# Performance work log

Measured on AMD Instinct MI355X. Metric: run time of the kernel, lower is better.

## Reference

```python
import jax, jax.numpy as jnp
import numpy as np
from math import log2

FPS = 100.0
MIN_BPM = 55.0
MAX_BPM = 215.0
NUM_TEMPI = 60
NUM_BEATS = 4
TRANS_LAMBDA = 100.0
OBS_LAMBDA = 16.0
NUM_FRAMES = 6000


def _intervals():
    mi = 60.0 * FPS / MAX_BPM
    ma = 60.0 * FPS / MIN_BPM
    iv = np.arange(round(mi), round(ma) + 1)
    if NUM_TEMPI < len(iv):
        n = NUM_TEMPI
        iv = np.zeros(0)
        while len(iv) < NUM_TEMPI:
            iv = np.unique(np.round(np.logspace(log2(mi), log2(ma), n, base=2)))
            n += 1
    return iv.astype(np.int64)


def _state_space():
    iv = _intervals()                      # (I,) tempo intervals in frames
    nsb = int(iv.sum())                    # states per beat
    first = np.concatenate([[0], np.cumsum(iv)[:-1]]).astype(np.int64)
    last = (np.cumsum(iv) - 1).astype(np.int64)
    pos_b = np.concatenate([np.arange(i) / float(i) for i in iv])
    positions = np.concatenate([pos_b + b for b in range(NUM_BEATS)])  # (S,)
    first_states = np.stack([first + b * nsb for b in range(NUM_BEATS)])  # (B,I)
    last_states = np.stack([last + b * nsb for b in range(NUM_BEATS)])    # (B,I)
    # exponential tempo transition (madmom exponential_transition, norm=True)
    ratio = iv[None, :].astype(np.float64) / iv[:, None].astype(np.float64)
    prob = np.exp(-TRANS_LAMBDA * np.abs(ratio - 1.0))
    prob[prob <= np.spacing(1)] = 0.0
    prob /= prob.sum(axis=1, keepdims=True)
    log_t = np.where(prob > 0, np.log(np.maximum(prob, 1e-300)), -1e30).astype(np.float32)
    log_trans = np.tile(log_t[None], (NUM_BEATS, 1, 1))  # same lambda per beat boundary
    prev_last = np.stack([last_states[(b - 1) % NUM_BEATS] for b in range(NUM_BEATS)])
    # observation pointers: 0 = no beat, 1 = beat, 2 = downbeat
    frac = positions % 1.0
    beat_idx = np.floor(positions).astype(np.int64)
    ptr = np.where(frac < 1.0 / OBS_LAMBDA, np.where(beat_idx == 0, 2, 1), 0)
    return first_states, prev_last, log_trans, ptr, nsb * NUM_BEATS


def setup_inputs() -> dict:
    key = jax.random.key(0)
    first_states, prev_last, log_trans, pointer, S = _state_space()
    # beat/downbeat activation probabilities; scaled so beat+downbeat < 1
    acts = jax.random.uniform(key, (NUM_FRAMES, 2), dtype=jnp.float32) * 0.45
    return {
        "activations": acts,
        "log_trans": jnp.asarray(log_trans),
        "prev_last": jnp.asarray(prev_last, dtype=jnp.int32),
        "first_states": jnp.asarray(first_states, dtype=jnp.int32),
        "pointer": jnp.asarray(pointer, dtype=jnp.int32),
        "num_states": S,
    }


def reference(activations, log_trans, prev_last, first_states, pointer, num_states):
    S = int(num_states)
    NEG = jnp.float32(-1e30)
    a_b = activations[:, 0]
    a_d = activations[:, 1]
    # log observation densities: [no-beat, beat, downbeat], shape (F, 3)
    dens = jnp.stack([
        jnp.log((1.0 - a_b - a_d) / (OBS_LAMBDA - 1.0)),
        jnp.log(a_b),
        jnp.log(a_d),
    ], axis=1)
    first_flat = first_states.reshape(-1)  # (B*I,)
    base_ptr = jnp.arange(S, dtype=jnp.int32) - 1  # default predecessor s-1

    def step(v, dens_t):
        # within-interval advance: state s comes from s-1 with prob 1
        v_shift = jnp.concatenate([jnp.full((1,), NEG, v.dtype), v[:-1]])
        # beat boundaries: first states of beat b from last states of beat b-1
        cand = v[prev_last]                      # (B, I)
        scores = cand[:, :, None] + log_trans    # (B, I_from, I_to)
        best = scores.max(axis=1).reshape(-1)    # (B*I,)
        arg = scores.argmax(axis=1)              # (B, I_to)
        bp_first = jnp.take_along_axis(prev_last, arg.astype(jnp.int32), axis=1).reshape(-1)
        ptr = base_ptr.at[first_flat].set(bp_first)
        v_new = v_shift.at[first_flat].set(best) + dens_t[pointer]
        return v_new, ptr

    v0 = jnp.full((S,), -jnp.log(jnp.float32(S)))  # uniform initial distribution
    v_final, bps = jax.lax.scan(step, v0, dens)    # bps: (F, S) backpointers
    last_state = jnp.argmax(v_final).astype(jnp.int32)
    logp = v_final[last_state]

    def back(s, bp_t):
        p = bp_t[s]
        return p, p

    _, earlier = jax.lax.scan(back, last_state, bps[1:], reverse=True)
    path = jnp.concatenate([earlier, last_state[None]])  # (F,) best state sequence
    return path, logp
```

## Files before the change

kernel.cpp:

```cpp
#include <hip/hip_runtime.h>
#include <stdint.h>


#define NB 4
#define KF 15
#define QW 16
#define NPMAX 256
#define NEGV -1.0e30f
#define CH 11

__device__ __forceinline__ float bf16u_to_f(uint16_t u) {
    union { uint32_t i; float f; } v; v.i = ((uint32_t)u) << 16; return v.f;
}
template<int CTRL>
__device__ __forceinline__ int dpp_i(int x) {
    return __builtin_amdgcn_update_dpp(0, x, CTRL, 0xF, 0xF, true);
}
template<int CTRL>
__device__ __forceinline__ float dpp_f(float x) {
    return __int_as_float(dpp_i<CTRL>(__float_as_int(x)));
}
__device__ __forceinline__ void load_acts(const void* p, int isbf, int t, float& a, float& d) {
    if (isbf) {
        const uint16_t* u = (const uint16_t*)p;
        uint32_t w = *(const uint32_t*)(u + 2 * t);
        a = bf16u_to_f((uint16_t)w); d = bf16u_to_f((uint16_t)(w >> 16));
    } else {
        const float2* f = (const float2*)p;
        float2 v = f[t]; a = v.x; d = v.y;
    }
}

__global__ __launch_bounds__(1024) void dbn_viterbi_v7(
    const void* __restrict__ acts_raw,
    const void* __restrict__ lt_raw,
    const int*  __restrict__ prev_last,
    const int*  __restrict__ first_states,
    float*      __restrict__ out,
    float*      __restrict__ ws_lastv,
    float*      __restrict__ ws_dens,
    int T, int S, int F)
{
    const int tid  = (int)threadIdx.x;
    const int NP   = NB * T;
    const int lane = tid & 63;
    const int wvx  = tid >> 6;

    __shared__ alignas(16) float lring[32 * 256];
    __shared__ alignas(16) float densr[64 * 4];
    __shared__ alignas(16) float bpr2[1024];
    __shared__ float bound2[32];
    __shared__ int   fsld[NPMAX];
    __shared__ int   plds[NPMAX];
    __shared__ int   pref[NPMAX + 1];
    __shared__ float wvs[16];
    __shared__ int   wss[16];
    __shared__ int   flag_s, mspan_s, dlo_s, dhi_s;

    if (tid == 0) {
        const uint16_t* au = (const uint16_t*)acts_raw;
        int bf = 1;
        for (int i = 0; i < 32; i++) {
            uint16_t e = au[2 * i];
            uint8_t h8 = (uint8_t)(e >> 8);
            if (!(e == 0 || (h8 >= 0x20 && h8 < 0x40))) bf = 0;
        }
        flag_s = bf; mspan_s = 0; dlo_s = 0x3FFFFFFF; dhi_s = -0x3FFFFFFF;
    }
    if (tid < NP) { fsld[tid] = first_states[tid]; plds[tid] = prev_last[tid]; }
    for (int i = tid; i < 32 * 256; i += 1024) lring[i] = NEGV;
    __syncthreads();
    const int isbf = flag_s;
    const int nsb  = S / NB;
    const uint16_t* lt_u = (const uint16_t*)lt_raw;
    const float*    lt_f = (const float*)lt_raw;

    for (int f = tid; f < F; f += 1024) {
        float ab, ad;
        load_acts(acts_raw, isbf, f, ab, ad);
        float4 r;
        r.x = logf(((1.0f - ab) - ad) / 15.0f);
        r.y = logf(ab);
        r.z = logf(ad);
        r.w = 0.0f;
        *(float4*)&ws_dens[f * 4] = r;
    }
    __threadfence();
    if (tid == 0) {
        int acc = 0;
        for (int g = 0; g < NP; g++) {
            int b = g / T, ib = g - b * T;
            int end = (ib + 1 < T) ? fsld[g + 1] : (b + 1) * nsb;
            int L = end - fsld[g];
            pref[g] = acc; acc += (L + KF - 1) / KF;
        }
        pref[NP] = acc;
    }
    __syncthreads();
    const int NT = pref[NP];
    const float vinit = -logf((float)S);
    const int WQ = NP >> 2, TQ = T >> 2;

    const bool act_u = (tid < NT);
    int g_own = 0, startg = 0, Lg = 1, sb = 0, lq = 0, kk_head = -1;
    bool is_last = false, pv2 = false, pred_is_head = false;
    if (act_u) {
        int lo = 0, hi = NP - 1;
        while (lo < hi) { int mid = (lo + hi + 1) >> 1; if (pref[mid] <= tid) lo = mid; else hi = mid - 1; }
        g_own = lo;
        int j = tid - pref[lo];
        int b = g_own / T, ib = g_own - b * T;
        startg = fsld[g_own];
        int end = (ib + 1 < T) ? fsld[g_own + 1] : (b + 1) * nsb;
        Lg = end - startg;
        int n = (Lg + KF - 1) / KF;
        sb = startg + Lg - KF * (n - j);
        is_last = (j == n - 1);
        lq = (b << 6) + ib;
        pv2 = (b == 0);
        int i0 = sb - startg;
        kk_head = (i0 <= 0) ? (-i0) : -1;
        pred_is_head = (i0 == 1);
    }
    bool hb[KF], hpp[KF];
    #pragma unroll
    for (int kk = 0; kk < KF; kk++) {
        int i = (sb - startg) + kk;
        hb[kk]  = act_u && (16 * i < Lg);
        hpp[kk] = act_u && (kk >= 1) && (i == 1);
    }

    const int g_a = tid >> 2, k4 = tid & 3;
    const bool act_g = (g_a < NP);
    int rowbase = 0, lo_b = 0, b_a = 0, j_a = 0, dsel_a = 1;
    if (act_g) {
        b_a = g_a / T; j_a = g_a - b_a * T;
        rowbase = ((b_a + 3) & 3) << 6;
        dsel_a = (b_a == 0) ? 2 : 1;
        int lo = T, hi = 0;
        for (int i = 0; i < T; i++) {
            int idx = (b_a * T + i) * T + j_a;
            float v = isbf ? bf16u_to_f(lt_u[idx]) : lt_f[idx];
            if (v > -1e29f) { if (i < lo) lo = i; hi = i; }
        }
        lo_b = lo;
        if (k4 == 0) {
            atomicMax(&mspan_s, hi - lo + 1);
            atomicMin(&dlo_s, lo - j_a);
            atomicMax(&dhi_s, hi - j_a);
        }
    }
    __syncthreads();

    float vreg[KF];
    #pragma unroll
    for (int kk = 0; kk < KF; kk++) vreg[kk] = vinit;
    if (act_u && is_last) lring[(31 << 8) + lq] = vinit;
    if (lane == 63) bound2[16 + wvx] = vinit;
    if (tid < 256) {
        bpr2[256 + tid]     = vinit;
        bpr2[512 + 2 * tid] = vinit;
        bpr2[513 + 2 * tid] = vinit;
    }
    if (tid < 64 && tid < F) {
        float4 r = *(const float4*)&ws_dens[tid * 4];
        *(float4*)&densr[tid * 4] = r;
    }
    __syncthreads();

    int rupt = dpp_i<0x134>(lane);
    int rdnt = dpp_i<0x13C>(lane);
    const bool dirok = (__builtin_amdgcn_readlane(rupt, 5) == 6) &&
                       (__builtin_amdgcn_readlane(rdnt, 5) == 4);
    const int  bwid  = dhi_s - dlo_s + 1;
    const bool rotok = dirok && (bwid >= 1) && (bwid <= 4 * CH) && (NB == 4);

    float patchF;

    if (rotok) {
        const int b_h    = wvx >> 1;
        const int hlf    = wvx & 1;
        const int rbh    = ((b_h + 3) & 3) << 6;
        const int base_d = dlo_s + 2 * CH * hlf;
        const int bT     = b_h * T;
        float ltr[2 * CH];
        if (wvx < 8) {
            #pragma unroll
            for (int u = 0; u < 2 * CH; u++) {
                int i = lane + base_d + u;
                float v = NEGV;
                if (lane < T && i >= 0 && i < T) {
                    int idx = (b_h * T + i) * T + lane;
                    v = isbf ? bf16u_to_f(lt_u[idx]) : lt_f[idx];
                }
                ltr[u] = v;
            }
        } else {
            #pragma unroll
            for (int u = 0; u < 2 * CH; u++) ltr[u] = NEGV;
        }
        float4 dd = *(const float4*)&densr[0];
        float4 ddp; ddp.x = 0.f; ddp.y = 0.f; ddp.z = 0.f; ddp.w = 0.f;

        for (int t = 0; t < F; t++) {
            if ((t & 15) == 0 && t >= 16 && lane < WQ) {
                int row = t - 16 + wvx;
                int c = lane, beat = c / TQ;
                float4 v4 = *(const float4*)&lring[((row & 31) << 8) + 4 * c + 4 * beat];
                *(float4*)&ws_lastv[(size_t)row * NP + 4 * c] = v4;
            }
            if (wvx == 15 && (t & 31) == 0 && t >= 32 && lane < 32) {
                int fr = t + 31 + lane;
                if (fr < F) {
                    float4 r = *(const float4*)&ws_dens[fr * 4];
                    *(float4*)&densr[(fr & 63) * 4] = r;
                }
            }
            float4 ddn = *(const float4*)&densr[((t + 1) & 63) << 2];

            if (wvx < 8) {
                const int rb = (((t + 31) & 31) << 8) + rbh;
                float r0 = lring[rb + ((lane + base_d) & 63)];
                float r1 = lring[rb + ((lane + base_d + CH) & 63)];
                float a0 = r0 + ltr[0];
                float a1 = r1 + ltr[CH];
                #pragma unroll
                for (int k2 = 1; k2 < CH; k2++) {
                    r0 = dpp_f<0x134>(r0);
                    r1 = dpp_f<0x134>(r1);
                    a0 = fmaxf(a0, r0 + ltr[k2]);
                    a1 = fmaxf(a1, r1 + ltr[CH + k2]);
                }
                float hm = fmaxf(a0, a1);
                if (lane < T) bpr2[((t & 1) << 9) + ((bT + lane) << 1) + hlf] = hm;
            }

            float sh = dpp_f<0x13C>(vreg[KF - 1]);
            float2 pp = *(const float2*)&bpr2[(((t + 1) & 1) << 9) + (g_own << 1)];
            float dprev  = pv2 ? ddp.z : ddp.y;
            float patchv = fmaxf(pp.x, pp.y) + dprev;
            float d0  = dd.x;
            float dpv = pv2 ? dd.z : dd.y;
            float inc = (lane == 0) ? bound2[(((t + 1) & 1) << 4) + ((wvx + 15) & 15)] : sh;
            inc = pred_is_head ? patchv : inc;
            #pragma unroll
            for (int kk = KF - 1; kk >= 0; kk--) {
                float prev = (kk == 0) ? inc : vreg[kk - 1];
                prev = hpp[kk] ? patchv : prev;
                float add = hb[kk] ? dpv : d0;
                vreg[kk] = prev + add;
            }
            if (act_u && is_last) lring[((t & 31) << 8) + lq] = vreg[KF - 1];
            if (lane == 63) bound2[((t & 1) << 4) + wvx] = vreg[KF - 1];

            ddp = dd; dd = ddn;
            asm volatile("s_waitcnt lgkmcnt(0)\n\ts_barrier" ::: "memory");
        }
        {
            float2 pf = *(const float2*)&bpr2[(((F - 1) & 1) << 9) + (g_own << 1)];
            patchF = fmaxf(pf.x, pf.y) + (pv2 ? ddp.z : ddp.y);
        }
    } else {
        const bool banded = (mspan_s <= 44);
        float ltreg[QW];
        #pragma unroll
        for (int u = 0; u < QW; u++) ltreg[u] = NEGV;
        int cb = 0;
        if (act_g) {
            if (banded) { cb = (lo_b & ~3) + 12 * k4; if (cb > 52) cb = 52; }
            else cb = 16 * k4;
            const int nu = banded ? 12 : 16;
            for (int u = 0; u < nu; u++) {
                int i = cb + u;
                if (i < T) {
                    int idx = (b_a * T + i) * T + j_a;
                    ltreg[u] = isbf ? bf16u_to_f(lt_u[idx]) : lt_f[idx];
                }
            }
        }

        for (int t = 0; t < F; t++) {
            if ((t & 15) == 0 && t >= 16 && lane < WQ) {
                int row = t - 16 + wvx;
                int c = lane, beat = c / TQ;
                float4 v4 = *(const float4*)&lring[((row & 31) << 8) + 4 * c + 4 * beat];
                *(float4*)&ws_lastv[(size_t)row * NP + 4 * c] = v4;
            }
            if (wvx == 15 && (t & 31) == 0 && t >= 32 && lane < 32) {
                int fr = t + 31 + lane;
                if (fr < F) {
                    float4 r = *(const float4*)&ws_dens[fr * 4];
                    *(float4*)&densr[(fr & 63) * 4] = r;
                }
            }

            if (act_g) {
                const float* rowp = &lring[(((t + 31) & 31) << 8) + rowbase + cb];
                float4 l0 = *(const float4*)(rowp + 0);
                float4 l1 = *(const float4*)(rowp + 4);
                float4 l2 = *(const float4*)(rowp + 8);
                float m0 = fmaxf(fmaxf(l0.x + ltreg[0], l0.y + ltreg[1]),
                                 fmaxf(l0.z + ltreg[2], l0.w + ltreg[3]));
                float m1 = fmaxf(fmaxf(l1.x + ltreg[4], l1.y + ltreg[5]),
                                 fmaxf(l1.z + ltreg[6], l1.w + ltreg[7]));
                float m2 = fmaxf(fmaxf(l2.x + ltreg[8], l2.y + ltreg[9]),
                                 fmaxf(l2.z + ltreg[10], l2.w + ltreg[11]));
                float mv = fmaxf(fmaxf(m0, m1), m2);
                if (!banded) {
                    float4 l3 = *(const float4*)(rowp + 12);
                    float m3 = fmaxf(fmaxf(l3.x + ltreg[12], l3.y + ltreg[13]),
                                     fmaxf(l3.z + ltreg[14], l3.w + ltreg[15]));
                    mv = fmaxf(mv, m3);
                }
                mv = fmaxf(mv, dpp_f<0xB1>(mv));
                mv = fmaxf(mv, dpp_f<0x4E>(mv));
                if (k4 == 0) bpr2[((t & 1) << 8) + g_a] = mv + densr[((t & 63) << 2) + dsel_a];
            }

            float sh = __shfl_up(vreg[KF - 1], 1, 64);
            float patchv = bpr2[(((t + 1) & 1) << 8) + g_own];
            int doff = (t & 63) << 2;
            float d0  = densr[doff];
            float dpv = densr[doff + (pv2 ? 2 : 1)];
            float inc = (lane == 0) ? bound2[(((t + 1) & 1) << 4) + ((wvx + 15) & 15)] : sh;
            inc = pred_is_head ? patchv : inc;
            #pragma unroll
            for (int kk = KF - 1; kk >= 0; kk--) {
                float prev = (kk == 0) ? inc : vreg[kk - 1];
                prev = hpp[kk] ? patchv : prev;
                float add = hb[kk] ? dpv : d0;
                vreg[kk] = prev + add;
            }
            if (act_u && is_last) lring[((t & 31) << 8) + lq] = vreg[KF - 1];
            if (lane == 63) bound2[((t & 1) << 4) + wvx] = vreg[KF - 1];

            __syncthreads();
        }
        patchF = bpr2[(((F - 1) & 1) << 8) + g_own];
    }

    {
        int t0 = (F - 1) & ~15;
        int row = t0 + wvx;
        if (row <= F - 2 && lane < WQ) {
            int c = lane, beat = c / TQ;
            float4 v4 = *(const float4*)&lring[((row & 31) << 8) + 4 * c + 4 * beat];
            *(float4*)&ws_lastv[(size_t)row * NP + 4 * c] = v4;
        }
        __threadfence();
    }

    float mv = -INFINITY; int ms = 0x7FFFFFFF;
    #pragma unroll
    for (int kk = 0; kk < KF; kk++) {
        int s = sb + kk;
        float v = (kk == kk_head) ? patchF : vreg[kk];
        if (act_u && s >= startg && v > mv) { mv = v; ms = s; }
    }
    #pragma unroll
    for (int d = 1; d < 64; d <<= 1) {
        float ov = __shfl_xor(mv, d, 64);
        int   os = __shfl_xor(ms, d, 64);
        if (ov > mv || (ov == mv && os < ms)) { mv = ov; ms = os; }
    }
    if (lane == 0) { wvs[wvx] = mv; wss[wvx] = ms; }
    __syncthreads();

    if (tid == 0) {
        float bm = -INFINITY; int bs = 0x7FFFFFFF;
        for (int w = 0; w < 16; w++) {
            if (wvs[w] > bm || (wvs[w] == bm && wss[w] < bs)) { bm = wvs[w]; bs = wss[w]; }
        }
        int s = bs;
        int t = F - 1;
        out[F - 1] = (float)s;
        while (t > 0) {
            int b = s / nsb;
            int lo = b * T, hi = b * T + T - 1;
            while (lo < hi) { int mid = (lo + hi + 1) >> 1; if (fsld[mid] <= s) lo = mid; else hi = mid - 1; }
            int p = lo;
            int run = s - fsld[p];
            if (run == 0) {
                int jt = p - b * T;
                int pb = (b + 3) & 3;
                const float* lrow = &ws_lastv[(size_t)(t - 1) * NP + pb * T];
                float bmv = -INFINITY; int ai = 0;
                for (int i = 0; i < T; i++) {
                    int idx = (b * T + i) * T + jt;
                    float ltv = isbf ? bf16u_to_f(lt_u[idx]) : lt_f[idx];
                    float sc = lrow[i] + ltv;
                    if (sc > bmv) { bmv = sc; ai = i; }
                }
                s = plds[b * T + ai];
                out[t - 1] = (float)s;
                t--;
            } else {
                int m = (run < t) ? run : t;
                for (int jj = 0; jj < m; jj++) out[t - 1 - jj] = (float)(s - 1 - jj);
                s -= m; t -= m;
            }
        }
        out[F] = bm;
    }
}

__global__ __launch_bounds__(1024) void dbn_viterbi_v2(
    const void* __restrict__ acts_raw, const void* __restrict__ lt_raw,
    const int* __restrict__ prev_last, const int* __restrict__ first_states,
    float* __restrict__ out, float* __restrict__ ws_lastv, float* __restrict__ ws_dens,
    int T, int S, int F)
{
    const int tid  = (int)threadIdx.x;
    const int NP   = NB * T;
    const int lane = tid & 63;
    const int wvx  = tid >> 6;

    __shared__ alignas(16) float lring[32 * 256];
    __shared__ alignas(16) float densr[64 * 4];
    __shared__ float bestv[NPMAX];
    __shared__ float bound[16];
    __shared__ int   fsld[NPMAX];
    __shared__ int   plds[NPMAX];
    __shared__ int   pref[NPMAX + 1];
    __shared__ float wvs[16];
    __shared__ int   wss[16];
    __shared__ int   flag_s, mspan_s;

    if (tid == 0) {
        const uint16_t* au = (const uint16_t*)acts_raw;
        int bf = 1;
        for (int i = 0; i < 32; i++) {
            uint16_t e = au[2 * i];
            uint8_t h8 = (uint8_t)(e >> 8);
            if (!(e == 0 || (h8 >= 0x20 && h8 < 0x40))) bf = 0;
        }
        flag_s = bf; mspan_s = 0;
    }
    if (tid < NP) { fsld[tid] = first_states[tid]; plds[tid] = prev_last[tid]; }
    for (int i = tid; i < 32 * 256; i += 1024) lring[i] = NEGV;
    __syncthreads();
    const int isbf = flag_s;
    const int nsb  = S / NB;
    const uint16_t* lt_u = (const uint16_t*)lt_raw;
    const float*    lt_f = (const float*)lt_raw;

    for (int f = tid; f < F; f += 1024) {
        float ab, ad;
        load_acts(acts_raw, isbf, f, ab, ad);
        float4 r;
        r.x = logf(((1.0f - ab) - ad) / 15.0f);
        r.y = logf(ab);
        r.z = logf(ad);
        r.w = 0.0f;
        *(float4*)&ws_dens[f * 4] = r;
    }
    __threadfence();
    if (tid == 0) {
        int acc = 0;
        for (int g = 0; g < NP; g++) {
            int b = g / T, ib = g - b * T;
            int end = (ib + 1 < T) ? fsld[g + 1] : (b + 1) * nsb;
            int L = end - fsld[g];
            pref[g] = acc; acc += (L + KF - 1) / KF;
        }
        pref[NP] = acc;
    }
    __syncthreads();
    const int NT = pref[NP];

    const bool act_u = (tid < NT);
    int g_own = 0, startg = 0, Lg = 1, sb = 0, lq = 0;
    bool is_last = false, pv2 = false;
    if (act_u) {
        int lo = 0, hi = NP - 1;
        while (lo < hi) { int mid = (lo + hi + 1) >> 1; if (pref[mid] <= tid) lo = mid; else hi = mid - 1; }
        g_own = lo;
        int j = tid - pref[lo];
        int b = g_own / T, ib = g_own - b * T;
        startg = fsld[g_own];
        int end = (ib + 1 < T) ? fsld[g_own + 1] : (b + 1) * nsb;
        Lg = end - startg;
        int n = (Lg + KF - 1) / KF;
        sb = startg + Lg - KF * (n - j);
        is_last = (j == n - 1);
        lq = (b << 6) + ib;
        pv2 = (b == 0);
    }
    bool hb[KF], hq[KF];
    #pragma unroll
    for (int kk = 0; kk < KF; kk++) {
        int i = sb + kk - startg;
        hq[kk] = act_u && (i <= 0);
        hb[kk] = act_u && (16 * i < Lg);
    }

    const int g_a = tid >> 2, k4 = tid & 3;
    const bool act_g = (g_a < NP);
    int rowbase = 0, lo_b = 0, b_a = 0, j_a = 0;
    if (act_g) {
        b_a = g_a / T; j_a = g_a - b_a * T;
        rowbase = ((b_a + 3) & 3) << 6;
        int lo = T, hi = 0;
        for (int i = 0; i < T; i++) {
            int idx = (b_a * T + i) * T + j_a;
            float v = isbf ? bf16u_to_f(lt_u[idx]) : lt_f[idx];
            if (v > -1e29f) { if (i < lo) lo = i; hi = i; }
        }
        lo_b = lo;
        if (k4 == 0) atomicMax(&mspan_s, hi - lo + 1);
    }
    __syncthreads();
    const bool banded = (mspan_s <= 44);
    float ltreg[QW];
    #pragma unroll
    for (int u = 0; u < QW; u++) ltreg[u] = NEGV;
    int cb = 0;
    if (act_g) {
        if (banded) { cb = (lo_b & ~3) + 12 * k4; if (cb > 52) cb = 52; }
        else cb = 16 * k4;
        const int nu = banded ? 12 : 16;
        for (int u = 0; u < nu; u++) {
            int i = cb + u;
            if (i < T) {
                int idx = (b_a * T + i) * T + j_a;
                ltreg[u] = isbf ? bf16u_to_f(lt_u[idx]) : lt_f[idx];
            }
        }
    }

    const float vinit = -logf((float)S);
    float vreg[KF];
    #pragma unroll
    for (int kk = 0; kk < KF; kk++) vreg[kk] = vinit;
    if (act_u && is_last) lring[(31 << 8) + lq] = vinit;
    if (lane == 63) bound[wvx] = vinit;
    float inc_pipe = vinit;
    if (tid < 64 && tid < F) {
        float4 r = *(const float4*)&ws_dens[tid * 4];
        *(float4*)&densr[tid * 4] = r;
    }
    const int WQ = NP >> 2, TQ = T >> 2;

    for (int t = 0; t < F; t++) {
        __syncthreads();
        const float* lvR = &lring[((t + 31) & 31) << 8];
        float inc_use = inc_pipe;
        if (lane == 0) inc_use = bound[(wvx + 15) & 15];

        if (wvx == 15) {
            if ((t & 31) == 0 && t >= 32 && lane < 32) {
                int fr = t + 32 + lane;
                if (fr < F) {
                    float4 r = *(const float4*)&ws_dens[fr * 4];
                    *(float4*)&densr[(fr & 63) * 4] = r;
                }
            }
            if ((t & 15) == 0 && t > 0 && lane < WQ) {
                int c = lane, beat = c / TQ;
                int srcoff = 4 * c + 4 * beat, t0 = t - 16;
                for (int r2 = 0; r2 < 16; r2++) {
                    int row = t0 + r2;
                    float4 v4 = *(const float4*)&lring[((row & 31) << 8) + srcoff];
                    *(float4*)&ws_lastv[(size_t)row * NP + 4 * c] = v4;
                }
            }
        } else if (act_g) {
            const float* rowp = lvR + rowbase + cb;
            float4 l0 = *(const float4*)(rowp + 0);
            float4 l1 = *(const float4*)(rowp + 4);
            float4 l2 = *(const float4*)(rowp + 8);
            float m0 = fmaxf(fmaxf(l0.x + ltreg[0], l0.y + ltreg[1]),
                             fmaxf(l0.z + ltreg[2], l0.w + ltreg[3]));
            float m1 = fmaxf(fmaxf(l1.x + ltreg[4], l1.y + ltreg[5]),
                             fmaxf(l1.z + ltreg[6], l1.w + ltreg[7]));
            float m2 = fmaxf(fmaxf(l2.x + ltreg[8], l2.y + ltreg[9]),
                             fmaxf(l2.z + ltreg[10], l2.w + ltreg[11]));
            float mv = fmaxf(fmaxf(m0, m1), m2);
            if (!banded) {
                float4 l3 = *(const float4*)(rowp + 12);
                float m3 = fmaxf(fmaxf(l3.x + ltreg[12], l3.y + ltreg[13]),
                                 fmaxf(l3.z + ltreg[14], l3.w + ltreg[15]));
                mv = fmaxf(mv, m3);
            }
            mv = fmaxf(mv, dpp_f<0xB1>(mv));
            mv = fmaxf(mv, dpp_f<0x4E>(mv));
            if (k4 == 0) bestv[g_a] = mv;
        }

        __syncthreads();
        int doff = (t & 63) << 2;
        float d0  = densr[doff];
        float dpv = densr[doff + (pv2 ? 2 : 1)];
        float bq  = bestv[g_own];
        #pragma unroll
        for (int kk = KF - 1; kk >= 0; kk--) {
            float prev = (kk == 0) ? inc_use : vreg[kk - 1];
            prev = hq[kk] ? bq : prev;
            float add = hb[kk] ? dpv : d0;
            vreg[kk] = prev + add;
        }
        if (act_u && is_last) lring[((t & 31) << 8) + lq] = vreg[KF - 1];
        if (lane == 63) bound[wvx] = vreg[KF - 1];
        inc_pipe = __shfl_up(vreg[KF - 1], 1, 64);
    }

    __syncthreads();
    if (wvx == 15 && lane < WQ) {
        int lastf = (F - 1) & ~15;
        int c = lane, beat = c / TQ;
        int srcoff = 4 * c + 4 * beat;
        for (int row = lastf; row <= F - 2; row++) {
            float4 v4 = *(const float4*)&lring[((row & 31) << 8) + srcoff];
            *(float4*)&ws_lastv[(size_t)row * NP + 4 * c] = v4;
        }
        __threadfence();
    }

    float mv = -INFINITY; int ms = 0x7FFFFFFF;
    #pragma unroll
    for (int kk = 0; kk < KF; kk++) {
        int s = sb + kk;
        bool valid = act_u && (s >= startg);
        float v = vreg[kk];
        if (valid && v > mv) { mv = v; ms = s; }
    }
    #pragma unroll
    for (int d = 1; d < 64; d <<= 1) {
        float ov = __shfl_xor(mv, d, 64);
        int   os = __shfl_xor(ms, d, 64);
        if (ov > mv || (ov == mv && os < ms)) { mv = ov; ms = os; }
    }
    if (lane == 0) { wvs[wvx] = mv; wss[wvx] = ms; }
    __syncthreads();

    if (tid == 0) {
        float bm = -INFINITY; int bs = 0x7FFFFFFF;
        for (int w = 0; w < 16; w++) {
            if (wvs[w] > bm || (wvs[w] == bm && wss[w] < bs)) { bm = wvs[w]; bs = wss[w]; }
        }
        int s = bs;
        int t = F - 1;
        out[F - 1] = (float)s;
        while (t > 0) {
            int b = s / nsb;
            int lo = b * T, hi = b * T + T - 1;
            while (lo < hi) { int mid = (lo + hi + 1) >> 1; if (fsld[mid] <= s) lo = mid; else hi = mid - 1; }
            int p = lo;
            int run = s - fsld[p];
            if (run == 0) {
                int jt = p - b * T;
                int pb = (b + 3) & 3;
                const float* lrow = &ws_lastv[(size_t)(t - 1) * NP + pb * T];
                float bmv = -INFINITY; int ai = 0;
                for (int i = 0; i < T; i++) {
                    int idx = (b * T + i) * T + jt;
                    float ltv = isbf ? bf16u_to_f(lt_u[idx]) : lt_f[idx];
                    float sc = lrow[i] + ltv;
                    if (sc > bmv) { bmv = sc; ai = i; }
                }
                s = plds[b * T + ai];
                out[t - 1] = (float)s;
                t--;
            } else {
                int m = (run < t) ? run : t;
                for (int jj = 0; jj < m; jj++) out[t - 1 - jj] = (float)(s - 1 - jj);
                s -= m; t -= m;
            }
        }
        out[F] = bm;
    }
}

extern "C" void kernel_launch(void* const* d_in, const int* in_sizes, int n_in,
                              void* d_out, int out_size, void* d_ws, size_t ws_size,
                              hipStream_t stream) {
    const int F  = in_sizes[0] / 2;
    const int NP = in_sizes[2];
    const int T  = NP / NB;
    const int S  = in_sizes[4];

    const size_t need = ((size_t)F * NP + 4 * (size_t)F) * 4;
    float* ws_lv = (float*)d_ws;
    float* ws_de = ws_lv + (size_t)F * NP;

    const bool base = ((T & 3) == 0) && (T <= 64) && (NP <= NPMAX) && (F >= 2)
                   && ((S % NB) == 0) && (S <= KF * 1024) && (ws_size >= need);

    if (base) {
        hipLaunchKernelGGL(dbn_viterbi_v7, dim3(1), dim3(1024), 0, stream,
                           d_in[0], d_in[1],
                           (const int*)d_in[2], (const int*)d_in[3],
                           (float*)d_out, ws_lv, ws_de, T, S, F);
    } else {
        hipLaunchKernelGGL(dbn_viterbi_v2, dim3(1), dim3(1024), 0, stream,
                           d_in[0], d_in[1],
                           (const int*)d_in[2], (const int*)d_in[3],
                           (float*)d_out, ws_lv, ws_de, T, S, F);
    }
}
```

Baseline: 6.066 ms.

## Split chain threads into head and plain groups to remove per-element selects

Thread-to-chunk assignment is reordered so chunks that touch a tempo's head states (needing patch/beat-density selects) go to low thread ids and plain shift-only chunks to the rest. Plain chunks run a simpler loop that adds only the no-beat density, with a new shared seam buffer passing values from head chunks to the first plain chunk. The beat-boundary max computation moves from waves 0-7 to waves 8-15, and the density prefetch to wave 3, so the two kinds of work sit on different waves. This is meant to cut per-element select cost and wave divergence, at the cost of one extra LDS exchange per step and a new minimum-length guard.

```diff
diff --git a/kernel.cpp b/kernel.cpp
--- a/kernel.cpp
+++ b/kernel.cpp
@@ -31,7 +31,7 @@
     }
 }
 
-__global__ __launch_bounds__(1024) void dbn_viterbi_v7(
+__global__ __launch_bounds__(1024) void dbn_viterbi_v8(
     const void* __restrict__ acts_raw,
     const void* __restrict__ lt_raw,
     const int*  __restrict__ prev_last,
@@ -49,13 +49,16 @@
     __shared__ alignas(16) float lring[32 * 256];
     __shared__ alignas(16) float densr[64 * 4];
     __shared__ alignas(16) float bpr2[1024];
+    __shared__ alignas(16) float hseam[512];
     __shared__ float bound2[32];
     __shared__ int   fsld[NPMAX];
     __shared__ int   plds[NPMAX];
-    __shared__ int   pref[NPMAX + 1];
+    __shared__ int   prefH[NPMAX + 1];
+    __shared__ int   prefP[NPMAX + 1];
+    __shared__ int   jp0a[NPMAX];
     __shared__ float wvs[16];
     __shared__ int   wss[16];
-    __shared__ int   flag_s, mspan_s, dlo_s, dhi_s;
+    __shared__ int   flag_s, mspan_s, dlo_s, dhi_s, ntot_s, minL_s;
 
     if (tid == 0) {
         const uint16_t* au = (const uint16_t*)acts_raw;
@@ -86,29 +89,52 @@
         *(float4*)&ws_dens[f * 4] = r;
     }
     __threadfence();
+
     if (tid == 0) {
-        int acc = 0;
+        int acc = 0, aH = 0, aP = 0, mnL = 1 << 30;
         for (int g = 0; g < NP; g++) {
             int b = g / T, ib = g - b * T;
             int end = (ib + 1 < T) ? fsld[g + 1] : (b + 1) * nsb;
             int L = end - fsld[g];
-            pref[g] = acc; acc += (L + KF - 1) / KF;
-        }
-        pref[NP] = acc;
-    }
-    __syncthreads();
-    const int NT = pref[NP];
+            if (L < mnL) mnL = L;
+            int n = (L + KF - 1) / KF;
+            int i01 = L - KF * (n - 1);
+            int jp0 = (n >= 2 && 16 * i01 < L) ? 2 : 1;
+            if (jp0 > n) jp0 = n;
+            jp0a[g] = jp0;
+            prefH[g] = aH; aH += jp0;
+            prefP[g] = aP; aP += n - jp0;
+            acc += n;
+        }
+        prefH[NP] = aH; prefP[NP] = aP;
+        ntot_s = acc; minL_s = mnL;
+    }
+    __syncthreads();
+    const int NH  = prefH[NP];
+    const int NTP = prefP[NP];
+    const int NT  = NH + NTP;
     const float vinit = -logf((float)S);
     const int WQ = NP >> 2, TQ = T >> 2;
 
     const bool act_u = (tid < NT);
     int g_own = 0, startg = 0, Lg = 1, sb = 0, lq = 0, kk_head = -1;
+    bool isH = false, firstP = false, wseam = false;
     bool is_last = false, pv2 = false, pred_is_head = false;
     if (act_u) {
-        int lo = 0, hi = NP - 1;
-        while (lo < hi) { int mid = (lo + hi + 1) >> 1; if (pref[mid] <= tid) lo = mid; else hi = mid - 1; }
-        g_own = lo;
-        int j = tid - pref[lo];
+        int j;
+        if (tid < NH) {
+            isH = true;
+            int lo = 0, hi = NP - 1;
+            while (lo < hi) { int mid = (lo + hi + 1) >> 1; if (prefH[mid] <= tid) lo = mid; else hi = mid - 1; }
+            g_own = lo;
+            j = tid - prefH[lo];
+        } else {
+            int p = tid - NH;
+            int lo = 0, hi = NP - 1;
+            while (lo < hi) { int mid = (lo + hi + 1) >> 1; if (prefP[mid] <= p) lo = mid; else hi = mid - 1; }
+            g_own = lo;
+            j = jp0a[lo] + (p - prefP[lo]);
+        }
         int b = g_own / T, ib = g_own - b * T;
         startg = fsld[g_own];
         int end = (ib + 1 < T) ? fsld[g_own + 1] : (b + 1) * nsb;
@@ -121,6 +147,8 @@
         int i0 = sb - startg;
         kk_head = (i0 <= 0) ? (-i0) : -1;
         pred_is_head = (i0 == 1);
+        firstP = (!isH) && (j == jp0a[g_own]);
+        wseam  = isH && (j == jp0a[g_own] - 1);
     }
     bool hb[KF], hpp[KF];
     #pragma unroll
@@ -161,6 +189,7 @@
         bpr2[256 + tid]     = vinit;
         bpr2[512 + 2 * tid] = vinit;
         bpr2[513 + 2 * tid] = vinit;
+        hseam[256 + tid]    = vinit;
     }
     if (tid < 64 && tid < F) {
         float4 r = *(const float4*)&ws_dens[tid * 4];
@@ -173,18 +202,19 @@
     const bool dirok = (__builtin_amdgcn_readlane(rupt, 5) == 6) &&
                        (__builtin_amdgcn_readlane(rdnt, 5) == 4);
     const int  bwid  = dhi_s - dlo_s + 1;
-    const bool rotok = dirok && (bwid >= 1) && (bwid <= 4 * CH) && (NB == 4);
-
-    float patchF;
-
-    if (rotok) {
-        const int b_h    = wvx >> 1;
-        const int hlf    = wvx & 1;
+    const bool pathok = dirok && (bwid >= 1) && (bwid <= 4 * CH) && (NB == 4)
+                     && (minL_s >= 17) && (NT <= 1024);
+
+    float patchF = NEGV;
+
+    if (pathok) {
+        const int b_h    = (wvx - 8) >> 1;
+        const int hlf    = (wvx - 8) & 1;
         const int rbh    = ((b_h + 3) & 3) << 6;
         const int base_d = dlo_s + 2 * CH * hlf;
         const int bT     = b_h * T;
         float ltr[2 * CH];
-        if (wvx < 8) {
+        if (wvx >= 8) {
             #pragma unroll
             for (int u = 0; u < 2 * CH; u++) {
                 int i = lane + base_d + u;
@@ -209,7 +239,7 @@
                 float4 v4 = *(const float4*)&lring[((row & 31) << 8) + 4 * c + 4 * beat];
                 *(float4*)&ws_lastv[(size_t)row * NP + 4 * c] = v4;
             }
-            if (wvx == 15 && (t & 31) == 0 && t >= 32 && lane < 32) {
+            if (wvx == 3 && (t & 31) == 0 && t >= 32 && lane < 32) {
                 int fr = t + 31 + lane;
                 if (fr < F) {
                     float4 r = *(const float4*)&ws_dens[fr * 4];
@@ -218,7 +248,7 @@
             }
             float4 ddn = *(const float4*)&densr[((t + 1) & 63) << 2];
 
-            if (wvx < 8) {
+            if (wvx >= 8) {
                 const int rb = (((t + 31) & 31) << 8) + rbh;
                 float r0 = lring[rb + ((lane + base_d) & 63)];
                 float r1 = lring[rb + ((lane + base_d + CH) & 63)];
@@ -235,28 +265,38 @@
                 if (lane < T) bpr2[((t & 1) << 9) + ((bT + lane) << 1) + hlf] = hm;
             }
 
-            float sh = dpp_f<0x13C>(vreg[KF - 1]);
-            float2 pp = *(const float2*)&bpr2[(((t + 1) & 1) << 9) + (g_own << 1)];
-            float dprev  = pv2 ? ddp.z : ddp.y;
-            float patchv = fmaxf(pp.x, pp.y) + dprev;
+            float sh  = dpp_f<0x13C>(vreg[KF - 1]);
             float d0  = dd.x;
-            float dpv = pv2 ? dd.z : dd.y;
             float inc = (lane == 0) ? bound2[(((t + 1) & 1) << 4) + ((wvx + 15) & 15)] : sh;
-            inc = pred_is_head ? patchv : inc;
-            #pragma unroll
-            for (int kk = KF - 1; kk >= 0; kk--) {
-                float prev = (kk == 0) ? inc : vreg[kk - 1];
-                prev = hpp[kk] ? patchv : prev;
-                float add = hb[kk] ? dpv : d0;
-                vreg[kk] = prev + add;
-            }
-            if (act_u && is_last) lring[((t & 31) << 8) + lq] = vreg[KF - 1];
+            if (isH) {
+                float2 pp = *(const float2*)&bpr2[(((t + 1) & 1) << 9) + (g_own << 1)];
+                float dprev  = pv2 ? ddp.z : ddp.y;
+                float patchv = fmaxf(pp.x, pp.y) + dprev;
+                float dpv = pv2 ? dd.z : dd.y;
+                float incH = pred_is_head ? patchv : inc;
+                #pragma unroll
+                for (int kk = KF - 1; kk >= 0; kk--) {
+                    float prev = (kk == 0) ? incH : vreg[kk - 1];
+                    prev = hpp[kk] ? patchv : prev;
+                    float add = hb[kk] ? dpv : d0;
+                    vreg[kk] = prev + add;
+                }
+                if (wseam) hseam[((t & 1) << 8) + g_own] = vreg[KF - 1];
+            } else {
+                float incP = firstP ? hseam[(((t + 1) & 1) << 8) + g_own] : inc;
+                #pragma unroll
+                for (int kk = KF - 1; kk >= 0; kk--) {
+                    float prev = (kk == 0) ? incP : vreg[kk - 1];
+                    vreg[kk] = prev + d0;
+                }
+                if (act_u && is_last) lring[((t & 31) << 8) + lq] = vreg[KF - 1];
+            }
             if (lane == 63) bound2[((t & 1) << 4) + wvx] = vreg[KF - 1];
 
             ddp = dd; dd = ddn;
             asm volatile("s_waitcnt lgkmcnt(0)\n\ts_barrier" ::: "memory");
         }
-        {
+        if (isH) {
             float2 pf = *(const float2*)&bpr2[(((F - 1) & 1) << 9) + (g_own << 1)];
             patchF = fmaxf(pf.x, pf.y) + (pv2 ? ddp.z : ddp.y);
         }
@@ -323,6 +363,7 @@
             float d0  = densr[doff];
             float dpv = densr[doff + (pv2 ? 2 : 1)];
             float inc = (lane == 0) ? bound2[(((t + 1) & 1) << 4) + ((wvx + 15) & 15)] : sh;
+            inc = firstP ? hseam[(((t + 1) & 1) << 8) + g_own] : inc;
             inc = pred_is_head ? patchv : inc;
             #pragma unroll
             for (int kk = KF - 1; kk >= 0; kk--) {
@@ -332,6 +373,7 @@
                 vreg[kk] = prev + add;
             }
             if (act_u && is_last) lring[((t & 31) << 8) + lq] = vreg[KF - 1];
+            if (wseam) hseam[((t & 1) << 8) + g_own] = vreg[KF - 1];
             if (lane == 63) bound2[((t & 1) << 4) + wvx] = vreg[KF - 1];
 
             __syncthreads();
@@ -687,7 +729,7 @@
                    && ((S % NB) == 0) && (S <= KF * 1024) && (ws_size >= need);
 
     if (base) {
-        hipLaunchKernelGGL(dbn_viterbi_v7, dim3(1), dim3(1024), 0, stream,
+        hipLaunchKernelGGL(dbn_viterbi_v8, dim3(1), dim3(1024), 0, stream,
                            d_in[0], d_in[1],
                            (const int*)d_in[2], (const int*)d_in[3],
                            (float*)d_out, ws_lv, ws_de, T, S, F);
```

Measured after the change: 6.944 ms. 14.5% more time.

## Block Viterbi forward into 8-frame chunks with tempo-packed wavefronts

Applied to the files above, without the earlier changes.

Restructures the single-block Viterbi forward pass so that each barrier interval advances eight frames instead of one. Beat-boundary maxima are computed ahead for a whole chunk, exploiting the minimum segment length of each tempo row. Tempo segments are bin-packed so each wavefront owns whole segments, which lets neighbours pass values through DPP shifts instead of cross-wave bound exchange. States per thread grow from 15 to 17. This aims to remove the per-frame __syncthreads latency on the serial recurrence, at the cost of more registers, extra lookahead arithmetic, and tighter preconditions with a fallback path.

```diff
diff --git a/kernel.cpp b/kernel.cpp
--- a/kernel.cpp
+++ b/kernel.cpp
@@ -4,6 +4,8 @@
 
 #define NB 4
 #define KF 15
+#define KFF 17
+#define BQ 8
 #define QW 16
 #define NPMAX 256
 #define NEGV -1.0e30f
@@ -31,7 +33,7 @@
     }
 }
 
-__global__ __launch_bounds__(1024) void dbn_viterbi_v7(
+__global__ __launch_bounds__(1024) void dbn_viterbi_v11(
     const void* __restrict__ acts_raw,
     const void* __restrict__ lt_raw,
     const int*  __restrict__ prev_last,
@@ -48,14 +50,15 @@
 
     __shared__ alignas(16) float lring[32 * 256];
     __shared__ alignas(16) float densr[64 * 4];
-    __shared__ alignas(16) float bpr2[1024];
-    __shared__ float bound2[32];
+    __shared__ alignas(16) float bpr2[8 * 512];
+    __shared__ float bound[16];
     __shared__ int   fsld[NPMAX];
     __shared__ int   plds[NPMAX];
-    __shared__ int   pref[NPMAX + 1];
+    __shared__ int   prefT[NPMAX + 1];
+    __shared__ unsigned char lag[1024], laj[1024];
     __shared__ float wvs[16];
     __shared__ int   wss[16];
-    __shared__ int   flag_s, mspan_s, dlo_s, dhi_s;
+    __shared__ int   flag_s, mspan_s, dlo_s, dhi_s, minL_s, packok_s;
 
     if (tid == 0) {
         const uint16_t* au = (const uint16_t*)acts_raw;
@@ -69,6 +72,7 @@
     }
     if (tid < NP) { fsld[tid] = first_states[tid]; plds[tid] = prev_last[tid]; }
     for (int i = tid; i < 32 * 256; i += 1024) lring[i] = NEGV;
+    lag[tid] = 255; laj[tid] = 0;
     __syncthreads();
     const int isbf = flag_s;
     const int nsb  = S / NB;
@@ -86,57 +90,64 @@
         *(float4*)&ws_dens[f * 4] = r;
     }
     __threadfence();
+
     if (tid == 0) {
-        int acc = 0;
+        int acc = 0, mnL = 1 << 30, pok = 1;
+        int nb0[64];
         for (int g = 0; g < NP; g++) {
             int b = g / T, ib = g - b * T;
             int end = (ib + 1 < T) ? fsld[g + 1] : (b + 1) * nsb;
             int L = end - fsld[g];
-            pref[g] = acc; acc += (L + KF - 1) / KF;
-        }
-        pref[NP] = acc;
-    }
-    __syncthreads();
-    const int NT = pref[NP];
-    const float vinit = -logf((float)S);
-    const int WQ = NP >> 2, TQ = T >> 2;
-
-    const bool act_u = (tid < NT);
-    int g_own = 0, startg = 0, Lg = 1, sb = 0, lq = 0, kk_head = -1;
-    bool is_last = false, pv2 = false, pred_is_head = false;
-    if (act_u) {
-        int lo = 0, hi = NP - 1;
-        while (lo < hi) { int mid = (lo + hi + 1) >> 1; if (pref[mid] <= tid) lo = mid; else hi = mid - 1; }
-        g_own = lo;
-        int j = tid - pref[lo];
-        int b = g_own / T, ib = g_own - b * T;
-        startg = fsld[g_own];
-        int end = (ib + 1 < T) ? fsld[g_own + 1] : (b + 1) * nsb;
-        Lg = end - startg;
-        int n = (Lg + KF - 1) / KF;
-        sb = startg + Lg - KF * (n - j);
-        is_last = (j == n - 1);
-        lq = (b << 6) + ib;
-        pv2 = (b == 0);
-        int i0 = sb - startg;
-        kk_head = (i0 <= 0) ? (-i0) : -1;
-        pred_is_head = (i0 == 1);
-    }
-    bool hb[KF], hpp[KF];
-    #pragma unroll
-    for (int kk = 0; kk < KF; kk++) {
-        int i = (sb - startg) + kk;
-        hb[kk]  = act_u && (16 * i < Lg);
-        hpp[kk] = act_u && (kk >= 1) && (i == 1);
+            if (L < mnL) mnL = L;
+            int n = (L + KFF - 1) / KFF;
+            prefT[g] = acc; acc += n;
+            if (b == 0) nb0[ib] = n;
+            else if (n != nb0[ib]) pok = 0;
+        }
+        prefT[NP] = acc;
+        if (T > 64) pok = 0;
+        unsigned char blist[4][64]; int bcnt[4] = {0,0,0,0}; int bfill[4] = {0,0,0,0};
+        if (pok) {
+            for (int nn = 64; nn >= 1; nn--) {
+                for (int ib = 0; ib < T; ib++) {
+                    if (nb0[ib] != nn) continue;
+                    int placed = 0;
+                    for (int x = 0; x < 4; x++) {
+                        if (bfill[x] + nn <= 64) {
+                            blist[x][bcnt[x]++] = (unsigned char)ib;
+                            bfill[x] += nn; placed = 1; break;
+                        }
+                    }
+                    if (!placed) { pok = 0; break; }
+                }
+                if (!pok) break;
+            }
+        }
+        if (pok) {
+            for (int b = 0; b < NB; b++) {
+                for (int x = 0; x < 4; x++) {
+                    int lc = 0;
+                    for (int q = 0; q < bcnt[x]; q++) {
+                        int ib = blist[x][q];
+                        int g = b * T + ib;
+                        for (int j = 0; j < nb0[ib]; j++) {
+                            lag[(4 * b + x) * 64 + lc] = (unsigned char)g;
+                            laj[(4 * b + x) * 64 + lc] = (unsigned char)j;
+                            lc++;
+                        }
+                    }
+                }
+            }
+        }
+        minL_s = mnL; packok_s = pok;
     }
 
     const int g_a = tid >> 2, k4 = tid & 3;
     const bool act_g = (g_a < NP);
-    int rowbase = 0, lo_b = 0, b_a = 0, j_a = 0, dsel_a = 1;
+    int rowbase = 0, lo_b = 0, b_a = 0, j_a = 0;
     if (act_g) {
         b_a = g_a / T; j_a = g_a - b_a * T;
         rowbase = ((b_a + 3) & 3) << 6;
-        dsel_a = (b_a == 0) ? 2 : 1;
         int lo = T, hi = 0;
         for (int i = 0; i < T; i++) {
             int idx = (b_a * T + i) * T + j_a;
@@ -152,32 +163,60 @@
     }
     __syncthreads();
 
-    float vreg[KF];
-    #pragma unroll
-    for (int kk = 0; kk < KF; kk++) vreg[kk] = vinit;
-    if (act_u && is_last) lring[(31 << 8) + lq] = vinit;
-    if (lane == 63) bound2[16 + wvx] = vinit;
-    if (tid < 256) {
-        bpr2[256 + tid]     = vinit;
-        bpr2[512 + 2 * tid] = vinit;
-        bpr2[513 + 2 * tid] = vinit;
-    }
+    const float vinit = -logf((float)S);
+    const int WQ = NP >> 2, TQ = T >> 2;
+    const int NT = prefT[NP];
+
+    if (tid < NP) lring[(31 << 8) + ((tid / T) << 6) + (tid % T)] = vinit;
     if (tid < 64 && tid < F) {
         float4 r = *(const float4*)&ws_dens[tid * 4];
         *(float4*)&densr[tid * 4] = r;
     }
-    __syncthreads();
 
     int rupt = dpp_i<0x134>(lane);
     int rdnt = dpp_i<0x13C>(lane);
     const bool dirok = (__builtin_amdgcn_readlane(rupt, 5) == 6) &&
                        (__builtin_amdgcn_readlane(rdnt, 5) == 4);
     const int  bwid  = dhi_s - dlo_s + 1;
-    const bool rotok = dirok && (bwid >= 1) && (bwid <= 4 * CH) && (NB == 4);
-
-    float patchF;
-
-    if (rotok) {
+    const bool pathok = dirok && (bwid >= 1) && (bwid <= 4 * CH) && (NB == 4)
+                     && packok_s && (minL_s >= 19) && ((F % BQ) == 0) && (F >= 2 * BQ)
+                     && ((T & 3) == 0) && (T <= 64) && (NP <= NPMAX);
+
+    bool  act_u = false, is_last = false, pv2 = false;
+    int   g_own = 0, startg = 0, sb = 0, lq = 0, kk_head = -1;
+    float patchF = NEGV;
+    float vreg[KFF];
+    #pragma unroll
+    for (int kk = 0; kk < KFF; kk++) vreg[kk] = vinit;
+
+    if (pathok) {
+        int gg = lag[tid];
+        act_u = (gg != 255);
+        bool pred_is_head = false;
+        int Lg = 1;
+        if (act_u) {
+            g_own = gg;
+            int b = g_own / T, ib = g_own - b * T;
+            startg = fsld[g_own];
+            int end = (ib + 1 < T) ? fsld[g_own + 1] : (b + 1) * nsb;
+            Lg = end - startg;
+            int n = (Lg + KFF - 1) / KFF;
+            int j = laj[tid];
+            sb = startg + Lg - KFF * (n - j);
+            is_last = (j == n - 1);
+            lq = (b << 6) + ib;
+            pv2 = (b == 0);
+            int i0 = sb - startg;
+            kk_head = (i0 <= 0) ? (-i0) : -1;
+            pred_is_head = (i0 == 1);
+        }
+        bool hb[KFF], hpp[KFF];
+        #pragma unroll
+        for (int kk = 0; kk < KFF; kk++) {
+            int i = (sb - startg) + kk;
+            hb[kk]  = act_u && (16 * i < Lg);
+            hpp[kk] = act_u && (kk >= 1) && (i == 1);
+        }
         const int b_h    = wvx >> 1;
         const int hlf    = wvx & 1;
         const int rbh    = ((b_h + 3) & 3) << 6;
@@ -199,27 +238,21 @@
             #pragma unroll
             for (int u = 0; u < 2 * CH; u++) ltr[u] = NEGV;
         }
-        float4 dd = *(const float4*)&densr[0];
-        float4 ddp; ddp.x = 0.f; ddp.y = 0.f; ddp.z = 0.f; ddp.w = 0.f;
-
-        for (int t = 0; t < F; t++) {
-            if ((t & 15) == 0 && t >= 16 && lane < WQ) {
-                int row = t - 16 + wvx;
-                int c = lane, beat = c / TQ;
-                float4 v4 = *(const float4*)&lring[((row & 31) << 8) + 4 * c + 4 * beat];
-                *(float4*)&ws_lastv[(size_t)row * NP + 4 * c] = v4;
-            }
-            if (wvx == 15 && (t & 31) == 0 && t >= 32 && lane < 32) {
-                int fr = t + 31 + lane;
-                if (fr < F) {
-                    float4 r = *(const float4*)&ws_dens[fr * 4];
-                    *(float4*)&densr[(fr & 63) * 4] = r;
-                }
-            }
-            float4 ddn = *(const float4*)&densr[((t + 1) & 63) << 2];
-
-            if (wvx < 8) {
-                const int rb = (((t + 31) & 31) << 8) + rbh;
+        if (tid < 512) bpr2[(7 << 9) + tid] = vinit;
+        __syncthreads();
+
+        if (act_u && is_last) {
+            float s = vinit;
+            #pragma unroll
+            for (int p = 0; p < BQ - 2; p++) {
+                s += densr[(p & 63) << 2];
+                lring[((p & 31) << 8) + lq] = s;
+            }
+        }
+        __syncthreads();
+        if (wvx < 8) {
+            for (int k = 0; k < BQ - 1; k++) {
+                const int rb = (((k - 1) & 31) << 8) + rbh;
                 float r0 = lring[rb + ((lane + base_d) & 63)];
                 float r1 = lring[rb + ((lane + base_d + CH) & 63)];
                 float a0 = r0 + ltr[0];
@@ -232,35 +265,123 @@
                     a1 = fmaxf(a1, r1 + ltr[CH + k2]);
                 }
                 float hm = fmaxf(a0, a1);
-                if (lane < T) bpr2[((t & 1) << 9) + ((bT + lane) << 1) + hlf] = hm;
-            }
-
-            float sh = dpp_f<0x13C>(vreg[KF - 1]);
-            float2 pp = *(const float2*)&bpr2[(((t + 1) & 1) << 9) + (g_own << 1)];
-            float dprev  = pv2 ? ddp.z : ddp.y;
-            float patchv = fmaxf(pp.x, pp.y) + dprev;
-            float d0  = dd.x;
-            float dpv = pv2 ? dd.z : dd.y;
-            float inc = (lane == 0) ? bound2[(((t + 1) & 1) << 4) + ((wvx + 15) & 15)] : sh;
-            inc = pred_is_head ? patchv : inc;
+                if (lane < T) bpr2[((k & 7) << 9) + ((bT + lane) << 1) + hlf] = hm;
+            }
+        }
+        __syncthreads();
+
+        for (int t = 0; t < F; t += BQ) {
+            if (t > 0 && wvx < 8 && lane < WQ) {
+                int row = t - 8 + wvx;
+                int c = lane, beat = c / TQ;
+                float4 v4 = *(const float4*)&lring[((row & 31) << 8) + 4 * c + 4 * beat];
+                *(float4*)&ws_lastv[(size_t)row * NP + 4 * c] = v4;
+            }
+            if (wvx == 15 && (t & 31) == 0 && t >= 32 && lane < 32) {
+                int fr = t + 31 + lane;
+                if (fr < F) {
+                    float4 r = *(const float4*)&ws_dens[fr * 4];
+                    *(float4*)&densr[(fr & 63) * 4] = r;
+                }
+            }
+            float d0p[BQ + 6], dpvp[BQ + 1];
             #pragma unroll
-            for (int kk = KF - 1; kk >= 0; kk--) {
-                float prev = (kk == 0) ? inc : vreg[kk - 1];
-                prev = hpp[kk] ? patchv : prev;
-                float add = hb[kk] ? dpv : d0;
-                vreg[kk] = prev + add;
-            }
-            if (act_u && is_last) lring[((t & 31) << 8) + lq] = vreg[KF - 1];
-            if (lane == 63) bound2[((t & 1) << 4) + wvx] = vreg[KF - 1];
-
-            ddp = dd; dd = ddn;
+            for (int u = 0; u <= BQ + 6; u++) {
+                float4 r = *(const float4*)&densr[((t - 1 + u) & 63) << 2];
+                if (u >= 1) d0p[u - 1] = r.x;
+                if (u <= BQ) dpvp[u] = pv2 ? r.z : r.y;
+            }
+            if (t == 0) dpvp[0] = 0.0f;
+
+            #pragma unroll
+            for (int k = 0; k < BQ; k++) {
+                float sh = dpp_f<0x13C>(vreg[KFF - 1]);
+                float2 pp = *(const float2*)&bpr2[(((t + k - 1) & 7) << 9) + (g_own << 1)];
+                float patchv = fmaxf(pp.x, pp.y) + dpvp[k];
+                float d0  = d0p[k];
+                float dpv = dpvp[k + 1];
+                float inc = pred_is_head ? patchv : sh;
+                #pragma unroll
+                for (int kk = KFF - 1; kk >= 0; kk--) {
+                    float prev = (kk == 0) ? inc : vreg[kk - 1];
+                    prev = hpp[kk] ? patchv : prev;
+                    float add = hb[kk] ? dpv : d0;
+                    vreg[kk] = prev + add;
+                }
+                if (act_u && is_last) lring[(((t + k) & 31) << 8) + lq] = vreg[KFF - 1];
+            }
+            if (act_u && is_last) {
+                #pragma unroll
+                for (int p = 0; p < BQ - 2; p++) {
+                    float s = vreg[KFF - 2 - p];
+                    #pragma unroll
+                    for (int u = 0; u <= p; u++) s += d0p[BQ + u];
+                    lring[(((t + BQ + p) & 31) << 8) + lq] = s;
+                }
+            }
             asm volatile("s_waitcnt lgkmcnt(0)\n\ts_barrier" ::: "memory");
+
+            if (wvx < 8) {
+                for (int k = 0; k < BQ; k++) {
+                    const int rb = (((t + BQ - 2 + k) & 31) << 8) + rbh;
+                    float r0 = lring[rb + ((lane + base_d) & 63)];
+                    float r1 = lring[rb + ((lane + base_d + CH) & 63)];
+                    float a0 = r0 + ltr[0];
+                    float a1 = r1 + ltr[CH];
+                    #pragma unroll
+                    for (int k2 = 1; k2 < CH; k2++) {
+                        r0 = dpp_f<0x134>(r0);
+                        r1 = dpp_f<0x134>(r1);
+                        a0 = fmaxf(a0, r0 + ltr[k2]);
+                        a1 = fmaxf(a1, r1 + ltr[CH + k2]);
+                    }
+                    float hm = fmaxf(a0, a1);
+                    if (lane < T) bpr2[(((t + BQ - 1 + k) & 7) << 9) + ((bT + lane) << 1) + hlf] = hm;
+                }
+            }
+            asm volatile("s_waitcnt lgkmcnt(0)\n\ts_barrier" ::: "memory");
         }
         {
-            float2 pf = *(const float2*)&bpr2[(((F - 1) & 1) << 9) + (g_own << 1)];
-            patchF = fmaxf(pf.x, pf.y) + (pv2 ? ddp.z : ddp.y);
+            float2 pf = *(const float2*)&bpr2[(((F - 1) & 7) << 9) + (g_own << 1)];
+            float dpr = densr[(((F - 1) & 63) << 2) + (pv2 ? 2 : 1)];
+            patchF = fmaxf(pf.x, pf.y) + dpr;
+        }
+        {
+            int row = F - 8 + wvx;
+            if (wvx < 8 && row <= F - 2 && lane < WQ) {
+                int c = lane, beat = c / TQ;
+                float4 v4 = *(const float4*)&lring[((row & 31) << 8) + 4 * c + 4 * beat];
+                *(float4*)&ws_lastv[(size_t)row * NP + 4 * c] = v4;
+            }
+            __threadfence();
         }
     } else {
+        act_u = (tid < NT) && (tid < 1024);
+        int Lg = 1; bool pv2f = false;
+        if (act_u) {
+            int lo = 0, hi = NP - 1;
+            while (lo < hi) { int mid = (lo + hi + 1) >> 1; if (prefT[mid] <= tid) lo = mid; else hi = mid - 1; }
+            g_own = lo;
+            int j = tid - prefT[lo];
+            int b = g_own / T, ib = g_own - b * T;
+            startg = fsld[g_own];
+            int end = (ib + 1 < T) ? fsld[g_own + 1] : (b + 1) * nsb;
+            Lg = end - startg;
+            int n = (Lg + KFF - 1) / KFF;
+            sb = startg + Lg - KFF * (n - j);
+            is_last = (j == n - 1);
+            lq = (b << 6) + ib;
+            pv2f = (b == 0);
+        }
+        pv2 = pv2f;
+        kk_head = -1;
+        bool hb[KFF], hq[KFF];
+        #pragma unroll
+        for (int kk = 0; kk < KFF; kk++) {
+            int i = sb + kk - startg;
+            hq[kk] = act_u && (i <= 0);
+            hb[kk] = act_u && (16 * i < Lg);
+        }
         const bool banded = (mspan_s <= 44);
         float ltreg[QW];
         #pragma unroll
@@ -278,24 +399,34 @@
                 }
             }
         }
+        if (lane == 63) bound[wvx] = vinit;
+        float inc_pipe = vinit;
 
         for (int t = 0; t < F; t++) {
-            if ((t & 15) == 0 && t >= 16 && lane < WQ) {
-                int row = t - 16 + wvx;
-                int c = lane, beat = c / TQ;
-                float4 v4 = *(const float4*)&lring[((row & 31) << 8) + 4 * c + 4 * beat];
-                *(float4*)&ws_lastv[(size_t)row * NP + 4 * c] = v4;
-            }
-            if (wvx == 15 && (t & 31) == 0 && t >= 32 && lane < 32) {
-                int fr = t + 31 + lane;
-                if (fr < F) {
-                    float4 r = *(const float4*)&ws_dens[fr * 4];
-                    *(float4*)&densr[(fr & 63) * 4] = r;
-                }
-            }
-
-            if (act_g) {
-                const float* rowp = &lring[(((t + 31) & 31) << 8) + rowbase + cb];
+            __syncthreads();
+            const float* lvR = &lring[((t + 31) & 31) << 8];
+            float inc_use = inc_pipe;
+            if (lane == 0) inc_use = bound[(wvx + 15) & 15];
+
+            if (wvx == 15) {
+                if ((t & 31) == 0 && t >= 32 && lane < 32) {
+                    int fr = t + 32 + lane;
+                    if (fr < F) {
+                        float4 r = *(const float4*)&ws_dens[fr * 4];
+                        *(float4*)&densr[(fr & 63) * 4] = r;
+                    }
+                }
+                if ((t & 15) == 0 && t > 0 && lane < WQ) {
+                    int c = lane, beat = c / TQ;
+                    int srcoff = 4 * c + 4 * beat, t0 = t - 16;
+                    for (int r2 = 0; r2 < 16; r2++) {
+                        int row = t0 + r2;
+                        float4 v4 = *(const float4*)&lring[((row & 31) << 8) + srcoff];
+                        *(float4*)&ws_lastv[(size_t)row * NP + 4 * c] = v4;
+                    }
+                }
+            } else if (act_g) {
+                const float* rowp = lvR + rowbase + cb;
                 float4 l0 = *(const float4*)(rowp + 0);
                 float4 l1 = *(const float4*)(rowp + 4);
                 float4 l2 = *(const float4*)(rowp + 8);
@@ -314,45 +445,42 @@
                 }
                 mv = fmaxf(mv, dpp_f<0xB1>(mv));
                 mv = fmaxf(mv, dpp_f<0x4E>(mv));
-                if (k4 == 0) bpr2[((t & 1) << 8) + g_a] = mv + densr[((t & 63) << 2) + dsel_a];
-            }
-
-            float sh = __shfl_up(vreg[KF - 1], 1, 64);
-            float patchv = bpr2[(((t + 1) & 1) << 8) + g_own];
+                if (k4 == 0) bpr2[g_a] = mv;
+            }
+
+            __syncthreads();
             int doff = (t & 63) << 2;
             float d0  = densr[doff];
             float dpv = densr[doff + (pv2 ? 2 : 1)];
-            float inc = (lane == 0) ? bound2[(((t + 1) & 1) << 4) + ((wvx + 15) & 15)] : sh;
-            inc = pred_is_head ? patchv : inc;
+            float bq  = bpr2[g_own];
             #pragma unroll
-            for (int kk = KF - 1; kk >= 0; kk--) {
-                float prev = (kk == 0) ? inc : vreg[kk - 1];
-                prev = hpp[kk] ? patchv : prev;
+            for (int kk = KFF - 1; kk >= 0; kk--) {
+                float prev = (kk == 0) ? inc_use : vreg[kk - 1];
+                prev = hq[kk] ? bq : prev;
                 float add = hb[kk] ? dpv : d0;
                 vreg[kk] = prev + add;
             }
-            if (act_u && is_last) lring[((t & 31) << 8) + lq] = vreg[KF - 1];
-            if (lane == 63) bound2[((t & 1) << 4) + wvx] = vreg[KF - 1];
-
-            __syncthreads();
-        }
-        patchF = bpr2[(((F - 1) & 1) << 8) + g_own];
-    }
-
-    {
-        int t0 = (F - 1) & ~15;
-        int row = t0 + wvx;
-        if (row <= F - 2 && lane < WQ) {
+            if (act_u && is_last) lring[((t & 31) << 8) + lq] = vreg[KFF - 1];
+            if (lane == 63) bound[wvx] = vreg[KFF - 1];
+            inc_pipe = __shfl_up(vreg[KFF - 1], 1, 64);
+        }
+
+        __syncthreads();
+        if (wvx == 15 && lane < WQ) {
+            int lastf = (F - 1) & ~15;
             int c = lane, beat = c / TQ;
-            float4 v4 = *(const float4*)&lring[((row & 31) << 8) + 4 * c + 4 * beat];
-            *(float4*)&ws_lastv[(size_t)row * NP + 4 * c] = v4;
-        }
-        __threadfence();
+            int srcoff = 4 * c + 4 * beat;
+            for (int row = lastf; row <= F - 2; row++) {
+                float4 v4 = *(const float4*)&lring[((row & 31) << 8) + srcoff];
+                *(float4*)&ws_lastv[(size_t)row * NP + 4 * c] = v4;
+            }
+            __threadfence();
+        }
     }
 
     float mv = -INFINITY; int ms = 0x7FFFFFFF;
     #pragma unroll
-    for (int kk = 0; kk < KF; kk++) {
+    for (int kk = 0; kk < KFF; kk++) {
         int s = sb + kk;
         float v = (kk == kk_head) ? patchF : vreg[kk];
         if (act_u && s >= startg && v > mv) { mv = v; ms = s; }
@@ -684,10 +812,10 @@
     float* ws_de = ws_lv + (size_t)F * NP;
 
     const bool base = ((T & 3) == 0) && (T <= 64) && (NP <= NPMAX) && (F >= 2)
-                   && ((S % NB) == 0) && (S <= KF * 1024) && (ws_size >= need);
+                   && ((S % NB) == 0) && (S <= KFF * 1024) && (ws_size >= need);
 
     if (base) {
-        hipLaunchKernelGGL(dbn_viterbi_v7, dim3(1), dim3(1024), 0, stream,
+        hipLaunchKernelGGL(dbn_viterbi_v11, dim3(1), dim3(1024), 0, stream,
                            d_in[0], d_in[1],
                            (const int*)d_in[2], (const int*)d_in[3],
                            (float*)d_out, ws_lv, ws_de, T, S, F);
```

Result: no change. 6.150 ms (+1.4%).
